# Kernel optimization log

Measured on AMD Instinct MI355X. Metric: run time of the kernel, lower is better.

## Reference

```python
import jax, jax.numpy as jnp
import numpy as np

B, C, N, M = 8, 128, 2048, 512

def setup_inputs() -> dict:
    key = jax.random.key(0)
    k1, k2, k3, k4 = jax.random.split(key, 4)
    scale = 1.0 / np.sqrt(C)
    x = jax.random.normal(k1, (B, C, N), dtype=jnp.float32)
    # conv1d with kernel size 1 and no bias == channel-mixing matmul, weight [C_out, C_in]
    Wq = jax.random.normal(k2, (C, C), dtype=jnp.float32) * scale
    Wk = jax.random.normal(k3, (C, C), dtype=jnp.float32) * scale
    Wv = jax.random.normal(k4, (C, C), dtype=jnp.float32) * scale
    return {"x": x, "Wq": Wq, "Wk": Wk, "Wv": Wv, "npts_ds": M}

def reference(x, Wq, Wk, Wv, npts_ds):
    # q,k,v: [B,C,N] via 1x1 conv == einsum over input channels
    q = jnp.einsum('oc,bcn->bon', Wq, x)
    k = jnp.einsum('oc,bcn->bon', Wk, x)
    v = jnp.einsum('oc,bcn->bon', Wv, x)
    # energy: [B,N,N] = q^T k (contract channel dim)
    energy = jnp.einsum('bcn,bcm->bnm', q, k)
    scale_factor = jnp.sqrt(jnp.asarray(q.shape[-2], dtype=energy.dtype))  # sqrt(C)
    attention = jax.nn.softmax(energy / scale_factor, axis=-1)  # [B,N,N]
    selection = jnp.sum(attention, axis=-2)  # [B,N] column sums
    _, idx = jax.lax.top_k(selection, npts_ds)  # [B,M]
    # gather selected attention rows: [B,M,N]
    scores = jnp.take_along_axis(attention, idx[:, :, None], axis=1)
    # weighted sum of values: [B,M,C]
    out = jnp.einsum('bmn,bcn->bcm', scores, v)  # [B,C,M]
    return out
```

## Files before the change

### kernel.cpp

```cpp
#include <hip/hip_runtime.h>
#include <math.h>

namespace {
constexpr int B = 8, C = 128, N = 2048, M = 512;
constexpr int NSPLIT = 8;
constexpr int MBLK = 16;
constexpr float INV_SQRT_C = 0.08838834764831845f;
}

typedef __attribute__((ext_vector_type(8))) short short8;
typedef __attribute__((ext_vector_type(16))) float f32x16;
typedef unsigned short ushort_t;
typedef unsigned int u32;

__device__ inline ushort_t f2bf(float f) {
  union { float f; u32 u; } a; a.f = f;
  u32 r = a.u + 0x7fffu + ((a.u >> 16) & 1u);
  return (ushort_t)(r >> 16);
}
__device__ inline float bf2f(ushort_t h) {
  union { u32 u; float f; } a; a.u = ((u32)h) << 16; return a.f;
}

__global__ __launch_bounds__(256) void qkv_kernel(
    const float* __restrict__ x, const float* __restrict__ Wq,
    const float* __restrict__ Wk, const float* __restrict__ Wv,
    ushort_t* __restrict__ split, ushort_t* __restrict__ vbf) {
  const size_t TERM = (size_t)B * N * C;
  int kc = blockIdx.x;
  int o0 = kc * 8;
  int n = blockIdx.y * 256 + threadIdx.x;
  int b = blockIdx.z;
  const float* xb = x + (size_t)b * C * N + n;
  float aq[8] = {}, ak[8] = {}, av[8] = {};
  #pragma unroll 4
  for (int c = 0; c < C; ++c) {
    float xv = xb[(size_t)c * N];
    #pragma unroll
    for (int j = 0; j < 8; ++j) {
      aq[j] = fmaf(Wq[(o0 + j) * C + c], xv, aq[j]);
      ak[j] = fmaf(Wk[(o0 + j) * C + c], xv, ak[j]);
      av[j] = fmaf(Wv[(o0 + j) * C + c], xv, av[j]);
    }
  }
  #pragma unroll
  for (int j = 0; j < 8; ++j)
    vbf[((size_t)b * C + o0 + j) * N + n] = f2bf(av[j]);
  size_t rowoff = ((size_t)b * 16 + kc) * (size_t)N * 8 + (size_t)n * 8;
  #pragma unroll
  for (int tt = 0; tt < 3; ++tt) {
    short8 qv, kv;
    #pragma unroll
    for (int j = 0; j < 8; ++j) {
      ushort_t h = f2bf(aq[j]); qv[j] = (short)h; aq[j] -= bf2f(h);
      h = f2bf(ak[j]);          kv[j] = (short)h; ak[j] -= bf2f(h);
    }
    *(short8*)&split[tt * TERM + rowoff]       = qv;
    *(short8*)&split[(3 + tt) * TERM + rowoff] = kv;
  }
}

__global__ __launch_bounds__(256) void energy_kernel(
    const ushort_t* __restrict__ split,
    float* __restrict__ Ae, float* __restrict__ rowpart) {
  __shared__ float red[128][64];
  __shared__ float red2[128][2];
  const size_t TERM = (size_t)B * N * C;
  const size_t ROW8 = (size_t)N * 8;
  int t = threadIdx.x;
  int lane = t & 63, w = t >> 6;
  int wn = w & 1, wm = w >> 1;
  int lin = blockIdx.y * 16 + blockIdx.x;
  int xcd = lin & 7, slot = lin >> 3;
  int st = xcd * 2 + (slot >> 4);
  int wi = slot & 15;
  int mb = (st & 3) * 4 + (wi & 3);
  int nb = (st >> 2) * 4 + (wi >> 2);
  int m0 = mb * 128, n0 = nb * 128, b = blockIdx.z;
  int lr = lane & 31, lq = lane >> 5;
  size_t kbase = ((size_t)b * 16 + lq) * ROW8;
  const ushort_t* Abase = split + kbase + (size_t)(n0 + wn * 64 + lr) * 8;
  const ushort_t* Bbase = split + 3 * TERM + kbase + (size_t)(m0 + wm * 64 + lr) * 8;
  f32x16 acc[2][2] = {};
  #pragma unroll
  for (int s = 0; s < 8; ++s) {
    size_t so = (size_t)s * 2 * ROW8;
    short8 aT[3][2], bT[3][2];
    #pragma unroll
    for (int tt = 0; tt < 3; ++tt)
      #pragma unroll
      for (int i = 0; i < 2; ++i) {
        aT[tt][i] = *(const short8*)(Abase + tt * TERM + so + i * 256);
        bT[tt][i] = *(const short8*)(Bbase + tt * TERM + so + i * 256);
      }
    #pragma unroll
    for (int mt = 0; mt < 2; ++mt)
      #pragma unroll
      for (int nt = 0; nt < 2; ++nt) {
        acc[mt][nt] = __builtin_amdgcn_mfma_f32_32x32x16_bf16(aT[0][mt], bT[0][nt], acc[mt][nt], 0, 0, 0);
        acc[mt][nt] = __builtin_amdgcn_mfma_f32_32x32x16_bf16(aT[1][mt], bT[0][nt], acc[mt][nt], 0, 0, 0);
        acc[mt][nt] = __builtin_amdgcn_mfma_f32_32x32x16_bf16(aT[0][mt], bT[1][nt], acc[mt][nt], 0, 0, 0);
        acc[mt][nt] = __builtin_amdgcn_mfma_f32_32x32x16_bf16(aT[2][mt], bT[0][nt], acc[mt][nt], 0, 0, 0);
        acc[mt][nt] = __builtin_amdgcn_mfma_f32_32x32x16_bf16(aT[1][mt], bT[1][nt], acc[mt][nt], 0, 0, 0);
        acc[mt][nt] = __builtin_amdgcn_mfma_f32_32x32x16_bf16(aT[0][mt], bT[2][nt], acc[mt][nt], 0, 0, 0);
      }
  }
  int lc = lr;
  #pragma unroll
  for (int mt = 0; mt < 2; ++mt) {
    #pragma unroll
    for (int reg = 0; reg < 16; ++reg) {
      int row = (reg & 3) + 8 * (reg >> 2) + 4 * lq;
      int rloc = wn * 64 + mt * 32 + row;
      float e0 = expf(acc[mt][0][reg] * INV_SQRT_C);
      float e1 = expf(acc[mt][1][reg] * INV_SQRT_C);
      float* pA = Ae + ((size_t)b * N + n0 + rloc) * N + m0 + wm * 64 + lc;
      pA[0] = e0; pA[32] = e1;
      red[rloc][wm * 32 + lc] = e0 + e1;
    }
  }
  __syncthreads();
  {
    int row = t >> 1, h = t & 1;
    float ssum = 0.f;
    #pragma unroll
    for (int j0 = 0; j0 < 32; ++j0) {
      int j = (j0 + (t & 31)) & 31;
      ssum += red[row][h * 32 + j];
    }
    red2[row][h] = ssum;
  }
  __syncthreads();
  if (t < 128)
    rowpart[(size_t)mb * (B * N) + b * N + n0 + t] = red2[t][0] + red2[t][1];
}

__global__ __launch_bounds__(256) void colsum_kernel(
    const float* __restrict__ Ae, const float* __restrict__ rowpart,
    float* __restrict__ selpart) {
  __shared__ float sinv[256];
  int t = threadIdx.x;
  int m = blockIdx.x * 256 + t;
  int nch = blockIdx.y, b = blockIdx.z;
  int n0 = nch * (N / 8);
  {
    int n = n0 + t;
    float s = 0.f;
    #pragma unroll
    for (int sl = 0; sl < MBLK; ++sl)
      s += rowpart[(size_t)sl * (B * N) + b * N + n];
    sinv[t] = 1.0f / s;
  }
  __syncthreads();
  const float* Ab = Ae + (size_t)b * N * N;
  float acc = 0.f;
  #pragma unroll 8
  for (int n = n0; n < n0 + N / 8; ++n)
    acc = fmaf(Ab[(size_t)n * N + m], sinv[n - n0], acc);
  selpart[(size_t)nch * (B * N) + b * N + m] = acc;
}

__global__ __launch_bounds__(256) void topk_kernel(
    const float* __restrict__ selpart, int* __restrict__ idx) {
  __shared__ float s[N];
  __shared__ int rsum[64][4];
  int b = blockIdx.y;
  int t = threadIdx.x;
  for (int i = t; i < N; i += 256) {
    float v_ = 0.f;
    #pragma unroll
    for (int nch = 0; nch < 8; ++nch)
      v_ += selpart[(size_t)nch * (B * N) + b * N + i];
    s[i] = v_;
  }
  __syncthreads();
  int i = blockIdx.x * 64 + (t & 63);
  int jc = t >> 6;
  float val = s[i];
  int r = 0;
  for (int j = jc * 512; j < jc * 512 + 512; ++j) {
    float sj = s[j];
    r += (sj > val || (sj == val && j < i)) ? 1 : 0;
  }
  rsum[t & 63][jc] = r;
  __syncthreads();
  if (t < 64) {
    int rank = rsum[t][0] + rsum[t][1] + rsum[t][2] + rsum[t][3];
    if (rank < M) idx[b * M + rank] = blockIdx.x * 64 + t;
  }
}

__global__ __launch_bounds__(256) void out_kernel(
    const float* __restrict__ Ae, const float* __restrict__ rowpart,
    const ushort_t* __restrict__ vbf, const int* __restrict__ idx,
    float* __restrict__ part) {
  __shared__ ushort_t sc[64][72];
  __shared__ ushort_t vt[128][72];
  __shared__ int ridx[64];
  __shared__ float rinv[64];
  int t = threadIdx.x;
  int m0 = blockIdx.x * 64;
  int ns = blockIdx.y;
  int b = blockIdx.z;
  if (t < 64) {
    int r = idx[b * M + m0 + t];
    ridx[t] = r;
    float s = 0.f;
    #pragma unroll
    for (int sl = 0; sl < MBLK; ++sl)
      s += rowpart[(size_t)sl * (B * N) + b * N + r];
    rinv[t] = 1.0f / s;
  }
  __syncthreads();
  int lane = t & 63, w = t >> 6;
  int wc = w & 1, wm = w >> 1;
  int lr = lane & 31, lq = lane >> 5;
  f32x16 acc[2] = {};
  int nbeg = ns * (N / NSPLIT);
  for (int kb = 0; kb < N / NSPLIT; kb += 64) {
    __syncthreads();
    #pragma unroll
    for (int it = 0; it < 16; ++it) {
      int ii = it * 256 + t;
      int r = ii >> 6, cn = ii & 63;
      float sv = Ae[((size_t)b * N + ridx[r]) * N + nbeg + kb + cn] * rinv[r];
      sc[r][cn] = f2bf(sv);
    }
    #pragma unroll
    for (int it = 0; it < 4; ++it) {
      int u = it * 256 + t;
      int r = u >> 3, seg = u & 7;
      *(short8*)&vt[r][seg * 8] =
          *(const short8*)&vbf[((size_t)b * C + r) * N + nbeg + kb + seg * 8];
    }
    __syncthreads();
    #pragma unroll
    for (int ks = 0; ks < 4; ++ks) {
      short8 bf_ = *(const short8*)&sc[wm * 32 + lr][ks * 16 + lq * 8];
      #pragma unroll
      for (int ct = 0; ct < 2; ++ct) {
        short8 af = *(const short8*)&vt[wc * 64 + ct * 32 + lr][ks * 16 + lq * 8];
        acc[ct] = __builtin_amdgcn_mfma_f32_32x32x16_bf16(af, bf_, acc[ct], 0, 0, 0);
      }
    }
  }
  float* pb = part + ((size_t)ns * B + b) * C * M;
  #pragma unroll
  for (int ct = 0; ct < 2; ++ct) {
    #pragma unroll
    for (int reg = 0; reg < 16; ++reg) {
      int crow = wc * 64 + ct * 32 + (reg & 3) + 8 * (reg >> 2) + 4 * lq;
      pb[(size_t)crow * M + m0 + wm * 32 + lr] = acc[ct][reg];
    }
  }
}

__global__ __launch_bounds__(256) void reduce_kernel(
    const float* __restrict__ part, float* __restrict__ out) {
  int i = (blockIdx.x * 256 + threadIdx.x) * 4;
  float4 a = make_float4(0.f, 0.f, 0.f, 0.f);
  #pragma unroll
  for (int ns = 0; ns < NSPLIT; ++ns) {
    float4 p = *(const float4*)&part[(size_t)ns * (B * C * M) + i];
    a.x += p.x; a.y += p.y; a.z += p.z; a.w += p.w;
  }
  *(float4*)&out[i] = a;
}

extern "C" void kernel_launch(void* const* d_in, const int* in_sizes, int n_in,
                              void* d_out, int out_size, void* d_ws, size_t ws_size,
                              hipStream_t stream) {
  const float* x  = (const float*)d_in[0];
  const float* Wq = (const float*)d_in[1];
  const float* Wk = (const float*)d_in[2];
  const float* Wv = (const float*)d_in[3];
  float* out = (float*)d_out;

  const size_t TSZ = (size_t)B * N * C;
  ushort_t* split = (ushort_t*)d_ws;
  ushort_t* vbf   = split + 6 * TSZ;
  float* Ae       = (float*)(vbf + TSZ);
  float* rowpart  = Ae + (size_t)B * N * N;
  float* selpart  = rowpart + (size_t)MBLK * B * N;
  int*   idx      = (int*)(selpart + (size_t)8 * B * N);
  float* part     = (float*)split;

  qkv_kernel<<<dim3(16, N / 256, B), 256, 0, stream>>>(x, Wq, Wk, Wv, split, vbf);
  energy_kernel<<<dim3(N / 128, N / 128, B), 256, 0, stream>>>(split, Ae, rowpart);
  colsum_kernel<<<dim3(N / 256, 8, B), 256, 0, stream>>>(Ae, rowpart, selpart);
  topk_kernel<<<dim3(N / 64, B), 256, 0, stream>>>(selpart, idx);
  out_kernel<<<dim3(M / 64, NSPLIT, B), 256, 0, stream>>>(Ae, rowpart, vbf, idx, part);
  reduce_kernel<<<dim3(B * C * M / 1024), 256, 0, stream>>>(part, out);
}
```

Measured before the change: 236.3 us.

## Recompute attention exponentials instead of materializing full energy matrix

Removes the B×N×N fp32 exponentiated energy buffer. colsum_kernel and out_kernel now recompute q·k tiles with split-bf16 MFMAs and apply exp on the fly. The colsum path reduces through an LDS tile, and the out kernel recomputes only the gathered rows for each chunk. This trades a 128 MB write plus two rereads of that buffer for roughly three times the energy matmul compute.

```diff
diff --git a/kernel.cpp b/kernel.cpp
--- a/kernel.cpp
+++ b/kernel.cpp
@@ -61,8 +61,7 @@
 }
 
 __global__ __launch_bounds__(256) void energy_kernel(
-    const ushort_t* __restrict__ split,
-    float* __restrict__ Ae, float* __restrict__ rowpart) {
+    const ushort_t* __restrict__ split, float* __restrict__ rowpart) {
   __shared__ float red[128][64];
   __shared__ float red2[128][2];
   const size_t TERM = (size_t)B * N * C;
@@ -114,8 +113,6 @@
       int rloc = wn * 64 + mt * 32 + row;
       float e0 = expf(acc[mt][0][reg] * INV_SQRT_C);
       float e1 = expf(acc[mt][1][reg] * INV_SQRT_C);
-      float* pA = Ae + ((size_t)b * N + n0 + rloc) * N + m0 + wm * 64 + lc;
-      pA[0] = e0; pA[32] = e1;
       red[rloc][wm * 32 + lc] = e0 + e1;
     }
   }
@@ -136,28 +133,79 @@
 }
 
 __global__ __launch_bounds__(256) void colsum_kernel(
-    const float* __restrict__ Ae, const float* __restrict__ rowpart,
+    const ushort_t* __restrict__ split, const float* __restrict__ rowpart,
     float* __restrict__ selpart) {
   __shared__ float sinv[256];
+  __shared__ float eL[128][128];
+  const size_t TERM = (size_t)B * N * C;
+  const size_t ROW8 = (size_t)N * 8;
   int t = threadIdx.x;
-  int m = blockIdx.x * 256 + t;
+  int lane = t & 63, w = t >> 6;
+  int wn = w & 1, wm = w >> 1;
+  int m0 = blockIdx.x * 128;
   int nch = blockIdx.y, b = blockIdx.z;
-  int n0 = nch * (N / 8);
+  int n0c = nch * 256;
+  int lr = lane & 31, lq = lane >> 5;
   {
-    int n = n0 + t;
+    int n = n0c + t;
     float s = 0.f;
     #pragma unroll
     for (int sl = 0; sl < MBLK; ++sl)
       s += rowpart[(size_t)sl * (B * N) + b * N + n];
     sinv[t] = 1.0f / s;
   }
-  __syncthreads();
-  const float* Ab = Ae + (size_t)b * N * N;
-  float acc = 0.f;
-  #pragma unroll 8
-  for (int n = n0; n < n0 + N / 8; ++n)
-    acc = fmaf(Ab[(size_t)n * N + m], sinv[n - n0], acc);
-  selpart[(size_t)nch * (B * N) + b * N + m] = acc;
+  size_t kbase = ((size_t)b * 16 + lq) * ROW8;
+  const ushort_t* Bbase = split + 3 * TERM + kbase + (size_t)(m0 + wm * 64 + lr) * 8;
+  float accs = 0.f;
+  for (int tile = 0; tile < 2; ++tile) {
+    int n0 = n0c + tile * 128;
+    const ushort_t* Abase = split + kbase + (size_t)(n0 + wn * 64 + lr) * 8;
+    f32x16 acc[2][2] = {};
+    #pragma unroll
+    for (int s = 0; s < 8; ++s) {
+      size_t so = (size_t)s * 2 * ROW8;
+      short8 aT[3][2], bT[3][2];
+      #pragma unroll
+      for (int tt = 0; tt < 3; ++tt)
+        #pragma unroll
+        for (int i = 0; i < 2; ++i) {
+          aT[tt][i] = *(const short8*)(Abase + tt * TERM + so + i * 256);
+          bT[tt][i] = *(const short8*)(Bbase + tt * TERM + so + i * 256);
+        }
+      #pragma unroll
+      for (int mt = 0; mt < 2; ++mt)
+        #pragma unroll
+        for (int nt = 0; nt < 2; ++nt) {
+          acc[mt][nt] = __builtin_amdgcn_mfma_f32_32x32x16_bf16(aT[0][mt], bT[0][nt], acc[mt][nt], 0, 0, 0);
+          acc[mt][nt] = __builtin_amdgcn_mfma_f32_32x32x16_bf16(aT[1][mt], bT[0][nt], acc[mt][nt], 0, 0, 0);
+          acc[mt][nt] = __builtin_amdgcn_mfma_f32_32x32x16_bf16(aT[0][mt], bT[1][nt], acc[mt][nt], 0, 0, 0);
+          acc[mt][nt] = __builtin_amdgcn_mfma_f32_32x32x16_bf16(aT[2][mt], bT[0][nt], acc[mt][nt], 0, 0, 0);
+          acc[mt][nt] = __builtin_amdgcn_mfma_f32_32x32x16_bf16(aT[1][mt], bT[1][nt], acc[mt][nt], 0, 0, 0);
+          acc[mt][nt] = __builtin_amdgcn_mfma_f32_32x32x16_bf16(aT[0][mt], bT[2][nt], acc[mt][nt], 0, 0, 0);
+        }
+    }
+    __syncthreads();
+    #pragma unroll
+    for (int mt = 0; mt < 2; ++mt) {
+      #pragma unroll
+      for (int reg = 0; reg < 16; ++reg) {
+        int row = (reg & 3) + 8 * (reg >> 2) + 4 * lq;
+        int rloc = wn * 64 + mt * 32 + row;
+        float e0 = expf(acc[mt][0][reg] * INV_SQRT_C);
+        float e1 = expf(acc[mt][1][reg] * INV_SQRT_C);
+        eL[rloc][wm * 64 + lr]      = e0;
+        eL[rloc][wm * 64 + lr + 32] = e1;
+      }
+    }
+    __syncthreads();
+    if (t < 128) {
+      #pragma unroll 8
+      for (int j = 0; j < 128; ++j)
+        accs = fmaf(eL[j][t], sinv[tile * 128 + j], accs);
+    }
+  }
+  if (t < 128)
+    selpart[(size_t)nch * (B * N) + b * N + m0 + t] = accs;
 }
 
 __global__ __launch_bounds__(256) void topk_kernel(
@@ -191,13 +239,15 @@
 }
 
 __global__ __launch_bounds__(256) void out_kernel(
-    const float* __restrict__ Ae, const float* __restrict__ rowpart,
+    const ushort_t* __restrict__ split, const float* __restrict__ rowpart,
     const ushort_t* __restrict__ vbf, const int* __restrict__ idx,
     float* __restrict__ part) {
   __shared__ ushort_t sc[64][72];
   __shared__ ushort_t vt[128][72];
   __shared__ int ridx[64];
   __shared__ float rinv[64];
+  const size_t TERM = (size_t)B * N * C;
+  const size_t ROW8 = (size_t)N * 8;
   int t = threadIdx.x;
   int m0 = blockIdx.x * 64;
   int ns = blockIdx.y;
@@ -214,24 +264,48 @@
   __syncthreads();
   int lane = t & 63, w = t >> 6;
   int wc = w & 1, wm = w >> 1;
+  int qr = w & 1, qc = w >> 1;
   int lr = lane & 31, lq = lane >> 5;
+  size_t kbase = ((size_t)b * 16 + lq) * ROW8;
+  int arow = ridx[qr * 32 + lr];
+  const ushort_t* Agat = split + kbase + (size_t)arow * 8;
   f32x16 acc[2] = {};
   int nbeg = ns * (N / NSPLIT);
   for (int kb = 0; kb < N / NSPLIT; kb += 64) {
     __syncthreads();
-    #pragma unroll
-    for (int it = 0; it < 16; ++it) {
-      int ii = it * 256 + t;
-      int r = ii >> 6, cn = ii & 63;
-      float sv = Ae[((size_t)b * N + ridx[r]) * N + nbeg + kb + cn] * rinv[r];
-      sc[r][cn] = f2bf(sv);
+    const ushort_t* Bg = split + 3 * TERM + kbase
+                       + (size_t)(nbeg + kb + qc * 32 + lr) * 8;
+    f32x16 aq = {};
+    #pragma unroll
+    for (int s = 0; s < 8; ++s) {
+      size_t so = (size_t)s * 2 * ROW8;
+      short8 aQ[3], bQ[3];
+      #pragma unroll
+      for (int tt = 0; tt < 3; ++tt) {
+        aQ[tt] = *(const short8*)(Agat + tt * TERM + so);
+        bQ[tt] = *(const short8*)(Bg + tt * TERM + so);
+      }
+      aq = __builtin_amdgcn_mfma_f32_32x32x16_bf16(aQ[0], bQ[0], aq, 0, 0, 0);
+      aq = __builtin_amdgcn_mfma_f32_32x32x16_bf16(aQ[1], bQ[0], aq, 0, 0, 0);
+      aq = __builtin_amdgcn_mfma_f32_32x32x16_bf16(aQ[0], bQ[1], aq, 0, 0, 0);
+      aq = __builtin_amdgcn_mfma_f32_32x32x16_bf16(aQ[2], bQ[0], aq, 0, 0, 0);
+      aq = __builtin_amdgcn_mfma_f32_32x32x16_bf16(aQ[1], bQ[1], aq, 0, 0, 0);
+      aq = __builtin_amdgcn_mfma_f32_32x32x16_bf16(aQ[0], bQ[2], aq, 0, 0, 0);
+    }
+    #pragma unroll
+    for (int reg = 0; reg < 16; ++reg) {
+      int rowt = (reg & 3) + 8 * (reg >> 2) + 4 * lq;
+      int rh = qr * 32 + rowt;
+      float e = expf(aq[reg] * INV_SQRT_C);
+      float sv = e * rinv[rh];
+      sc[rh][qc * 32 + lr] = f2bf(sv);
     }
     #pragma unroll
     for (int it = 0; it < 4; ++it) {
       int u = it * 256 + t;
-      int r = u >> 3, seg = u & 7;
-      *(short8*)&vt[r][seg * 8] =
-          *(const short8*)&vbf[((size_t)b * C + r) * N + nbeg + kb + seg * 8];
+      int r2 = u >> 3, seg = u & 7;
+      *(short8*)&vt[r2][seg * 8] =
+          *(const short8*)&vbf[((size_t)b * C + r2) * N + nbeg + kb + seg * 8];
     }
     __syncthreads();
     #pragma unroll
@@ -279,16 +353,16 @@
   const size_t TSZ = (size_t)B * N * C;
   ushort_t* split = (ushort_t*)d_ws;
   ushort_t* vbf   = split + 6 * TSZ;
-  float* Ae       = (float*)(vbf + TSZ);
-  float* rowpart  = Ae + (size_t)B * N * N;
+  float* bigslot  = (float*)(vbf + TSZ);
+  float* part     = bigslot;
+  float* rowpart  = bigslot + (size_t)B * N * N;
   float* selpart  = rowpart + (size_t)MBLK * B * N;
   int*   idx      = (int*)(selpart + (size_t)8 * B * N);
-  float* part     = (float*)split;
 
   qkv_kernel<<<dim3(16, N / 256, B), 256, 0, stream>>>(x, Wq, Wk, Wv, split, vbf);
-  energy_kernel<<<dim3(N / 128, N / 128, B), 256, 0, stream>>>(split, Ae, rowpart);
-  colsum_kernel<<<dim3(N / 256, 8, B), 256, 0, stream>>>(Ae, rowpart, selpart);
+  energy_kernel<<<dim3(N / 128, N / 128, B), 256, 0, stream>>>(split, rowpart);
+  colsum_kernel<<<dim3(N / 128, 8, B), 256, 0, stream>>>(split, rowpart, selpart);
   topk_kernel<<<dim3(N / 64, B), 256, 0, stream>>>(selpart, idx);
-  out_kernel<<<dim3(M / 64, NSPLIT, B), 256, 0, stream>>>(Ae, rowpart, vbf, idx, part);
+  out_kernel<<<dim3(M / 64, NSPLIT, B), 256, 0, stream>>>(split, rowpart, vbf, idx, part);
   reduce_kernel<<<dim3(B * C * M / 1024), 256, 0, stream>>>(part, out);
 }
```

Result: slower. 288.4 us (+22.1%).
